# Kernel optimization log

Measured on AMD Instinct MI355X. Metric: run time of the kernel, lower is better.

## Reference

```python
import jax, jax.numpy as jnp
import numpy as np

# module config (matches init_kwargs)
SLICE_W, SLICE_H = 32, 32
STRIDE, WIDTH_INIT = 8, 8
EMBED_DIM = 512
B, H, W = 64, 32, 4096
PAD = (SLICE_W - WIDTH_INIT) // 2  # 12, width padding with constant value 1.0


def setup_inputs() -> dict:
    key = jax.random.key(0)
    k1, k2, k3, k4, k5 = jax.random.split(key, 5)
    u = lambda k, s: jax.random.uniform(k, s, jnp.float32, -0.08, 0.08)
    return {
        "images": jax.random.normal(k1, (B, 1, H, W), jnp.float32),
        "conv_w": u(k2, (1, 1, 3, 3)),          # Conv2d(1,1,3x3) weight (OIHW)
        "conv_b": u(k3, (1,)),
        "lin_w": u(k4, (SLICE_W * SLICE_H, EMBED_DIM)),  # bridge Linear, stored [in,out]
        "lin_b": u(k5, (EMBED_DIM,)),
    }


def reference(images, conv_w, conv_b, lin_w, lin_b):
    b = images.shape[0]
    # pad width with constant 1 (F.pad(..., 'constant', 1))
    padded = jnp.pad(images, ((0, 0), (0, 0), (0, 0), (PAD, PAD)), constant_values=1.0)
    # vectorized replacement of the python loop over stride positions
    starts = np.arange(0, W - 1, STRIDE)               # [S] static
    S = starts.shape[0]                                # 512
    idx = starts[:, None] + np.arange(SLICE_W)[None, :]  # [S, slice_w]
    sl = padded[:, :, :, idx]                          # [B,1,H,S,slice_w]
    sl = jnp.transpose(sl, (0, 3, 1, 2, 4))            # [B,S,1,H,slice_w]
    x = sl.reshape(b * S, 1, H, SLICE_W)               # pixels
    # embedder: Conv2d(1,1,k=3,pad=1) + ReLU
    y = jax.lax.conv_general_dilated(x, conv_w, (1, 1), ((1, 1), (1, 1)))
    y = jax.nn.relu(y + conv_b[None, :, None, None])
    # bridge: Linear(slice_w*slice_h -> embed_dim)
    flat = y.reshape(b * S, H * SLICE_W)
    out = flat @ lin_w + lin_b
    return out.reshape(b, S, EMBED_DIM)
```

## Files before the change

kernel.cpp:

```cpp
#include <hip/hip_runtime.h>
#include <cstdint>
#include <cstddef>

typedef unsigned short u16;
typedef unsigned int   u32;
typedef __attribute__((ext_vector_type(4))) float  f32x4;
typedef __attribute__((ext_vector_type(2))) float  f32x2;
typedef __attribute__((ext_vector_type(2))) u32    u32x2;
typedef __attribute__((ext_vector_type(8))) __bf16 bf16x8;

#define PSW   1056
#define ASTR  72
#define CFW   4128
#define WIN   2080

#define WS_BT  0u
#define WS_CF  1048576u
#define WS_AB  (1048576u + 16908288u)
#define WS_NEED (1048576u + 16908288u + 4194304u)

static __device__ __forceinline__ float b2f(u32 u) {
  union { u32 i; float f; } c; c.i = u << 16; return c.f;
}
static __device__ __forceinline__ u16 f2b(float f) {
  union { float f; u32 i; } c; c.f = f;
  return (u16)((c.i + 0x7FFFu + ((c.i >> 16) & 1u)) >> 16);
}

static __device__ __forceinline__ void gl_lds16(const void* g, void* l) {
  __builtin_amdgcn_global_load_lds(
      (__attribute__((address_space(1))) unsigned int*)(void*)g,
      (__attribute__((address_space(3))) unsigned int*)l, 16, 0, 0);
}
static __device__ __forceinline__ void gl_lds4(const void* g, void* l) {
  __builtin_amdgcn_global_load_lds(
      (__attribute__((address_space(1))) unsigned int*)(void*)g,
      (__attribute__((address_space(3))) unsigned int*)l, 4, 0, 0);
}

__global__ __launch_bounds__(256) void transpose_w(const float* __restrict__ lw,
                                                   u16* __restrict__ bt) {
  __shared__ u16 tile[64][65];
  const int t  = threadIdx.x;
  const int c  = t & 63, r0 = t >> 6;
  const int n0 = blockIdx.x * 64;
  const int k0 = blockIdx.y * 64;
#pragma unroll
  for (int rr = 0; rr < 16; ++rr) {
    const int r = r0 * 16 + rr;
    tile[r][c] = f2b(lw[(size_t)(k0 + r) * 512 + n0 + c]);
  }
  __syncthreads();
#pragma unroll
  for (int rr = 0; rr < 16; ++rr) {
    const int r = r0 * 16 + rr;
    bt[(size_t)(n0 + r) * 1024 + k0 + c] = tile[c][r];
  }
}

__global__ __launch_bounds__(512) void prep2(
    const float* __restrict__ img, const float* __restrict__ cw,
    const float* __restrict__ cb, u16* __restrict__ cf, u32* __restrict__ ab,
    const float* __restrict__ lw, u16* __restrict__ bt)
{
  __shared__ __align__(16) float RING[4 * WIN];
  const int t  = threadIdx.x;
  const int id = blockIdx.x;

  if (id >= 512) {
    u16* tile = (u16*)&RING[0];
    const int c = t & 63, r0 = t >> 6;
    for (int q = 0; q < 16; ++q) {
      const int T  = (id - 512) * 16 + q;
      const int n0 = (T & 7) << 6, k0 = (T >> 3) << 6;
      __syncthreads();
#pragma unroll
      for (int rr = 0; rr < 8; ++rr) {
        const int r = r0 * 8 + rr;
        tile[r * 65 + c] = f2b(lw[(size_t)(k0 + r) * 512 + n0 + c]);
      }
      __syncthreads();
#pragma unroll
      for (int rr = 0; rr < 8; ++rr) {
        const int r = r0 * 8 + rr;
        bt[(size_t)(n0 + r) * 1024 + k0 + c] = tile[c * 65 + r];
      }
    }
    return;
  }

  const int b  = id >> 3, sub = id & 7;
  const int ch = sub & 1, hq = sub >> 1;
  const int h0 = hq << 3;
  const int col0   = ch ? 2032 : 0;
  const int wstart = ch ? 0 : 16;
  const float* imgb = img + (size_t)b * 32 * 4096;

  float w9[9];
#pragma unroll
  for (int q = 0; q < 9; ++q) w9[q] = cw[q];
  const float bias = cb[0];

  auto STAGE = [&](int i2) {
    float* sp = RING + (i2 & 3) * WIN;
    const int hh = h0 - 1 + i2;
    if (hh >= 0 && hh <= 31) {
      const float* src = imgb + (ptrdiff_t)hh * 4096 + col0;
      gl_lds16(src + 4 * t, sp + wstart + ((t >> 6) << 8));
      if (t < 4) gl_lds16(src + 2048 + 4 * t, sp + wstart + 2048);
      if (ch == 0) { if (t < 16) sp[t] = (t < 4) ? 0.0f : 1.0f; }
      else         { if (t < 16) sp[2064 + t] = (t < 12) ? 1.0f : 0.0f; }
    } else {
      *(f32x4*)(sp + (t << 2)) = (f32x4)0.0f;
      if (t < 8) *(f32x4*)(sp + 2048 + (t << 2)) = (f32x4)0.0f;
    }
  };

  STAGE(0); STAGE(1); STAGE(2);
  __syncthreads();

#pragma unroll 1
  for (int it = 0; it < 8; ++it) {
    if (it < 7) STAGE(3 + it);
    const int h = h0 + it;
    const float* R0 = RING + ((it)     & 3) * WIN;
    const float* R1 = RING + ((it + 1) & 3) * WIN;
    const float* R2 = RING + ((it + 2) & 3) * WIN;
    u16* cfrow = cf + (size_t)(b * 32 + h) * CFW;

    f32x4 aa0, aa1, aa2;
    auto CONV4 = [&](int tl, bool exp) {
      const int w4 = tl << 2;
      const f32x4 a0 = *(const f32x4*)(R0 + w4), b0 = *(const f32x4*)(R0 + w4 + 4);
      const float c0 = R0[w4 + 8];
      const f32x4 a1 = *(const f32x4*)(R1 + w4), b1 = *(const f32x4*)(R1 + w4 + 4);
      const float c1 = R1[w4 + 8];
      const f32x4 a2 = *(const f32x4*)(R2 + w4), b2 = *(const f32x4*)(R2 + w4 + 4);
      const float c2 = R2[w4 + 8];
      float o0 = bias, o1 = bias, o2 = bias, o3 = bias;
      o0 += w9[0] * a0.w + w9[1] * b0.x + w9[2] * b0.y;
      o1 += w9[0] * b0.x + w9[1] * b0.y + w9[2] * b0.z;
      o2 += w9[0] * b0.y + w9[1] * b0.z + w9[2] * b0.w;
      o3 += w9[0] * b0.z + w9[1] * b0.w + w9[2] * c0;
      o0 += w9[3] * a1.w + w9[4] * b1.x + w9[5] * b1.y;
      o1 += w9[3] * b1.x + w9[4] * b1.y + w9[5] * b1.z;
      o2 += w9[3] * b1.y + w9[4] * b1.z + w9[5] * b1.w;
      o3 += w9[3] * b1.z + w9[4] * b1.w + w9[5] * c1;
      o0 += w9[6] * a2.w + w9[7] * b2.x + w9[8] * b2.y;
      o1 += w9[6] * b2.x + w9[7] * b2.y + w9[8] * b2.z;
      o2 += w9[6] * b2.y + w9[7] * b2.z + w9[8] * b2.w;
      o3 += w9[6] * b2.z + w9[7] * b2.w + w9[8] * c2;
      u32x2 pk;
      pk.x = (u32)f2b(fmaxf(o0, 0.f)) | ((u32)f2b(fmaxf(o1, 0.f)) << 16);
      pk.y = (u32)f2b(fmaxf(o2, 0.f)) | ((u32)f2b(fmaxf(o3, 0.f)) << 16);
      *(u32x2*)(cfrow + (ch << 11) + (tl << 2)) = pk;
      if (exp) { aa0 = a0; aa1 = a1; aa2 = a2; }
    };

    CONV4(t, true);
    if (ch == 1) {
      if (t < 6) CONV4(512 + t, false);
      if (t == 0) { u32x2 z; z.x = 0u; z.y = 0u; *(u32x2*)(cfrow + 4120) = z; }
    }

    u16* abh = (u16*)ab + (size_t)(b * 32 + h) * 1024;
    if (t & 1) {
      const int j = t >> 1;
      float v = bias;
      v += w9[1] * aa0.x + w9[2] * aa0.y;
      v += w9[4] * aa1.x + w9[5] * aa1.y;
      v += w9[7] * aa2.x + w9[8] * aa2.y;
      abh[((ch << 8) + j) << 1] = f2b(fmaxf(v, 0.f));
    } else if (t >= 8) {
      const int j = (t - 8) >> 1;
      float v = bias;
      v += w9[0] * aa0.z + w9[1] * aa0.w;
      v += w9[3] * aa1.z + w9[4] * aa1.w;
      v += w9[6] * aa2.z + w9[7] * aa2.w;
      abh[(((ch << 8) + j) << 1) | 1] = f2b(fmaxf(v, 0.f));
    } else {
      const int j = 252 + (t >> 1);
      const int wq = 8 * j + 34;
      const f32x2 u0 = *(const f32x2*)(R0 + wq);
      const f32x2 u1 = *(const f32x2*)(R1 + wq);
      const f32x2 u2 = *(const f32x2*)(R2 + wq);
      float v = bias;
      v += w9[0] * u0.x + w9[1] * u0.y;
      v += w9[3] * u1.x + w9[4] * u1.y;
      v += w9[6] * u2.x + w9[7] * u2.y;
      abh[(((ch << 8) + j) << 1) | 1] = f2b(fmaxf(v, 0.f));
    }
    __syncthreads();
  }
}

__global__ __launch_bounds__(256) void gemm_k2(
    const u16* __restrict__ cf, const u32* __restrict__ ab,
    const u16* __restrict__ bt, const float* __restrict__ lb,
    float* __restrict__ out)
{
  __shared__ __align__(16) char sm[2176 + 512 + 16384];
  u16* Ps   = (u16*)sm;
  u32* Ab32 = (u32*)(sm + 2176);
  u16* Bs   = (u16*)(sm + 2688);
  float* Cs = (float*)sm;

  const int t  = threadIdx.x;
  const int orig = blockIdx.y * 4 + blockIdx.x;
  const int wg   = ((orig & 7) << 8) + (orig >> 3);
  const int nt = wg & 3, mt = wg >> 2;
  const int b  = mt >> 3, sg = mt & 7;
  const int n0 = nt << 7;
  const int w  = t >> 6, i = t & 63;
  const int wr = w >> 1, wc = w & 1;
  const int lq = i >> 4, lr = i & 15;

  const int cB = (i & 7) ^ ((i >> 3) & 7);
  const u16* btp = bt + (size_t)(n0 + (w << 5) + (i >> 3)) * 1024 + (cB << 3);
  u16* BsW = Bs + (w << 11);

  const int rP  = (t >= 68) ? 1 : 0;
  const int ccP = t - 68 * rP;
  const u16* cfp = cf + (size_t)(b * 32 + rP) * CFW + (sg << 9) + (ccP << 3);
  u16* PsW = (u16*)((char*)Ps + (w << 10));

  const u32* abp = ab + (size_t)(b * 32 + (t >> 6)) * 512 + (sg << 6) + (t & 63);
  u32* AbW = Ab32 + (w << 6);

  f32x4 acc[2][4];
#pragma unroll
  for (int a = 0; a < 2; ++a)
#pragma unroll
    for (int c = 0; c < 4; ++c) acc[a][c] = (f32x4)0.0f;

  for (int kk = 0; kk < 16; ++kk) {
    __syncthreads();
    gl_lds16(btp,              BsW);
    gl_lds16(btp +  8 * 1024,  BsW + 512);
    gl_lds16(btp + 16 * 1024,  BsW + 1024);
    gl_lds16(btp + 24 * 1024,  BsW + 1536);
    if (t < 136) gl_lds16(cfp, PsW);
    if (t < 128) gl_lds4(abp, AbW);
    btp += 64; cfp += 2 * CFW; abp += 1024;
    __syncthreads();

#pragma unroll
    for (int kc = 0; kc < 2; ++kc) {
      const int bswz = (((kc << 2) + lq) ^ (lr & 7)) << 3;
      bf16x8 af[2], bfv[4];
#pragma unroll
      for (int im = 0; im < 2; ++im) {
        const int ml = wr * 32 + im * 16 + lr;
        af[im] = __builtin_bit_cast(bf16x8,
            *(const uint4*)(Ps + kc * 544 + ((ml + lq) << 3)));
        const u32 a32 = Ab32[kc * 64 + ml];
        union { u16 u; __bf16 h; } lo, hi;
        lo.u = (u16)(a32 & 0xffffu); hi.u = (u16)(a32 >> 16);
        if (lq == 0) af[im][0] = lo.h;
        if (lq == 3) af[im][7] = hi.h;
      }
#pragma unroll
      for (int jn = 0; jn < 4; ++jn) {
        const int n = wc * 64 + jn * 16 + lr;
        bfv[jn] = __builtin_bit_cast(bf16x8, *(const uint4*)(Bs + (n << 6) + bswz));
      }
#pragma unroll
      for (int im = 0; im < 2; ++im)
#pragma unroll
        for (int jn = 0; jn < 4; ++jn)
          acc[im][jn] = __builtin_amdgcn_mfma_f32_16x16x32_bf16(
              af[im], bfv[jn], acc[im][jn], 0, 0, 0);
    }
  }

  float lbv[4];
#pragma unroll
  for (int jn = 0; jn < 4; ++jn) lbv[jn] = lb[n0 + wc * 64 + jn * 16 + lr];

  const int erow = t >> 3, ecol = (t & 7) << 4;
  const int grow_base = (mt << 6) + ((erow >> 4) * 32) + (erow & 15);

#pragma unroll
  for (int im = 0; im < 2; ++im) {
    __syncthreads();
#pragma unroll
    for (int jn = 0; jn < 4; ++jn) {
      const int cl = wc * 64 + jn * 16 + lr;
#pragma unroll
      for (int r = 0; r < 4; ++r)
        Cs[(wr * 16 + lq * 4 + r) * 132 + cl] = acc[im][jn][r] + lbv[jn];
    }
    __syncthreads();
    const size_t grow = (size_t)(grow_base + im * 16);
    float* orow = out + grow * 512 + n0 + ecol;
    const float* crow = Cs + erow * 132 + ecol;
#pragma unroll
    for (int p = 0; p < 4; ++p)
      *(f32x4*)(orow + p * 4) = *(const f32x4*)(crow + p * 4);
  }
}

__global__ __launch_bounds__(256) void fused_fallback(
    const float* __restrict__ img, const float* __restrict__ cw,
    const float* __restrict__ cb, const u16* __restrict__ bt,
    const float* __restrict__ lb, float* __restrict__ out)
{
  __shared__ __align__(16) u16 Ps[4 * PSW];
  __shared__ __align__(16) u16 As[128 * ASTR];
  __shared__ __align__(16) u16 Bs[128 * ASTR];
  const int t = threadIdx.x, nt = blockIdx.x, mt = blockIdx.y;
  const int b = mt >> 2, s0 = (mt & 3) << 7, X0 = s0 << 3, n0 = nt << 7;
  const float* imgb = img + (size_t)b * 32 * 4096;
  float cwf[9];
#pragma unroll
  for (int q = 0; q < 9; ++q) cwf[q] = cw[q];
  const float bias = cb[0];
  const int wv = t >> 6, l = t & 63;
  const int wr = wv >> 1, wc = wv & 1, lq = l >> 4, lr = l & 15;
  const int sl = t >> 1, hsel = t & 1;
  f32x4 acc[4][4];
#pragma unroll
  for (int a = 0; a < 4; ++a)
#pragma unroll
    for (int c = 0; c < 4; ++c) acc[a][c] = (f32x4)0.0f;
  for (int kk = 0; kk < 16; ++kk) {
    const int h0 = kk << 1;
    __syncthreads();
    uint4 bsv[4];
#pragma unroll
    for (int p = 0; p < 4; ++p) {
      const int idx8 = t + (p << 8);
      const int n = idx8 >> 3, k8 = idx8 & 7;
      bsv[p] = *(const uint4*)(bt + (size_t)(n0 + n) * 1024 + (kk << 6) + (k8 << 3));
    }
    for (int idx = t; idx < 4 * PSW; idx += 256) {
      const int r = idx / PSW, xi = idx - r * PSW;
      const int h = h0 - 1 + r, x = X0 - 1 + xi;
      u16 v = 0;
      if (h >= 0 && h < 32 && x >= 0 && x < 4120)
        v = (x < 12 || x >= 4108) ? (u16)0x3F80 : f2b(imgb[h * 4096 + (x - 12)]);
      Ps[idx] = v;
    }
    __syncthreads();
    {
      const int pbase = (sl << 3);
#pragma unroll
      for (int wb = 0; wb < 32; wb += 16) {
        float o[16];
#pragma unroll
        for (int j = 0; j < 16; ++j) o[j] = bias;
#pragma unroll
        for (int dr = 0; dr < 3; ++dr) {
          const u16* p = Ps + (hsel + dr) * PSW + pbase + wb;
          const uint4 va = *(const uint4*)p;
          const uint4 vb = *(const uint4*)(p + 8);
          const u32   vc = *(const u32*)(p + 16);
          float win[18];
          win[0] = b2f(va.x & 0xffffu); win[1] = b2f(va.x >> 16);
          win[2] = b2f(va.y & 0xffffu); win[3] = b2f(va.y >> 16);
          win[4] = b2f(va.z & 0xffffu); win[5] = b2f(va.z >> 16);
          win[6] = b2f(va.w & 0xffffu); win[7] = b2f(va.w >> 16);
          win[8] = b2f(vb.x & 0xffffu); win[9] = b2f(vb.x >> 16);
          win[10] = b2f(vb.y & 0xffffu); win[11] = b2f(vb.y >> 16);
          win[12] = b2f(vb.z & 0xffffu); win[13] = b2f(vb.z >> 16);
          win[14] = b2f(vb.w & 0xffffu); win[15] = b2f(vb.w >> 16);
          win[16] = b2f(vc & 0xffffu);   win[17] = b2f(vc >> 16);
          if (wb == 0) win[0] = 0.f; else win[17] = 0.f;
          const float w0 = cwf[dr * 3], w1 = cwf[dr * 3 + 1], w2 = cwf[dr * 3 + 2];
#pragma unroll
          for (int j = 0; j < 16; ++j)
            o[j] += w0 * win[j] + w1 * win[j + 1] + w2 * win[j + 2];
        }
        u32 pk[8];
#pragma unroll
        for (int q = 0; q < 8; ++q)
          pk[q] = (u32)f2b(fmaxf(o[2 * q], 0.f)) | ((u32)f2b(fmaxf(o[2 * q + 1], 0.f)) << 16);
        uint4* dst = (uint4*)(As + sl * ASTR + (hsel << 5) + wb);
        dst[0] = make_uint4(pk[0], pk[1], pk[2], pk[3]);
        dst[1] = make_uint4(pk[4], pk[5], pk[6], pk[7]);
      }
    }
#pragma unroll
    for (int p = 0; p < 4; ++p) {
      const int idx8 = t + (p << 8);
      const int n = idx8 >> 3, k8 = idx8 & 7;
      *(uint4*)(Bs + n * ASTR + (k8 << 3)) = bsv[p];
    }
    __syncthreads();
#pragma unroll
    for (int kc = 0; kc < 2; ++kc) {
      const int ko = (kc << 5) + (lq << 3);
      bf16x8 af[4], bfv[4];
#pragma unroll
      for (int im = 0; im < 4; ++im)
        af[im] = __builtin_bit_cast(bf16x8,
            *(const uint4*)(As + (wr * 64 + im * 16 + lr) * ASTR + ko));
#pragma unroll
      for (int jn = 0; jn < 4; ++jn)
        bfv[jn] = __builtin_bit_cast(bf16x8,
            *(const uint4*)(Bs + (wc * 64 + jn * 16 + lr) * ASTR + ko));
#pragma unroll
      for (int im = 0; im < 4; ++im)
#pragma unroll
        for (int jn = 0; jn < 4; ++jn)
          acc[im][jn] = __builtin_amdgcn_mfma_f32_16x16x32_bf16(
              af[im], bfv[jn], acc[im][jn], 0, 0, 0);
    }
  }
#pragma unroll
  for (int jn = 0; jn < 4; ++jn) {
    const int col = n0 + wc * 64 + jn * 16 + lr;
    const float lbv = lb[col];
#pragma unroll
    for (int im = 0; im < 4; ++im) {
      const int row0 = (mt << 7) + wr * 64 + im * 16 + (lq << 2);
#pragma unroll
      for (int r = 0; r < 4; ++r)
        out[(size_t)(row0 + r) * 512 + col] = acc[im][jn][r] + lbv;
    }
  }
}

extern "C" void kernel_launch(void* const* d_in, const int* in_sizes, int n_in,
                              void* d_out, int out_size, void* d_ws, size_t ws_size,
                              hipStream_t stream) {
  const float* img = (const float*)d_in[0];
  const float* cw  = (const float*)d_in[1];
  const float* cb  = (const float*)d_in[2];
  const float* lw  = (const float*)d_in[3];
  const float* lb  = (const float*)d_in[4];
  float* out = (float*)d_out;

  u16* btw = (u16*)((char*)d_ws + WS_BT);

  if (ws_size >= WS_NEED) {
    u16* cfp = (u16*)((char*)d_ws + WS_CF);
    u32* abp = (u32*)((char*)d_ws + WS_AB);
    prep2<<<dim3(520), 512, 0, stream>>>(img, cw, cb, cfp, abp, lw, btw);
    gemm_k2<<<dim3(4, 512), 256, 0, stream>>>(cfp, abp, btw, lb, out);
  } else {
    transpose_w<<<dim3(8, 16), 256, 0, stream>>>(lw, btw);
    fused_fallback<<<dim3(4, 256), 256, 0, stream>>>(img, cw, cb, btw, lb, out);
  }
}
```

Before: 153.9 us.

## Replace LDS ring-buffered conv prep with one-row-per-block direct global loads

The prep kernel no longer stages image rows through a four-slot LDS ring with async global-to-LDS loads and per-row barriers. Instead each 256-thread block computes a single output row, and every thread reads its 3x16 input window straight from global memory with vector loads. This gives far more, smaller blocks (2056 instead of 520), removes the barrier-bound pipeline, and computes the boundary-column outputs directly. The cost is redundant input reads across neighbouring rows, which now rely on the cache, plus per-element padding logic at the edges.

New measurement: 219.8 us. 1.43x slower.

```diff
diff --git a/kernel.cpp b/kernel.cpp
--- a/kernel.cpp
+++ b/kernel.cpp
@@ -12,7 +12,6 @@
 #define PSW   1056
 #define ASTR  72
 #define CFW   4128
-#define WIN   2080
 
 #define WS_BT  0u
 #define WS_CF  1048576u
@@ -58,139 +57,108 @@
   }
 }
 
-__global__ __launch_bounds__(512) void prep2(
+__global__ __launch_bounds__(256) void prep3(
     const float* __restrict__ img, const float* __restrict__ cw,
     const float* __restrict__ cb, u16* __restrict__ cf, u32* __restrict__ ab,
     const float* __restrict__ lw, u16* __restrict__ bt)
 {
-  __shared__ __align__(16) float RING[4 * WIN];
+  __shared__ __align__(16) u16 tile[64 * 65];
   const int t  = threadIdx.x;
   const int id = blockIdx.x;
 
-  if (id >= 512) {
-    u16* tile = (u16*)&RING[0];
+  if (id >= 2048) {
     const int c = t & 63, r0 = t >> 6;
     for (int q = 0; q < 16; ++q) {
-      const int T  = (id - 512) * 16 + q;
+      const int T  = (id - 2048) * 16 + q;
       const int n0 = (T & 7) << 6, k0 = (T >> 3) << 6;
       __syncthreads();
 #pragma unroll
-      for (int rr = 0; rr < 8; ++rr) {
-        const int r = r0 * 8 + rr;
+      for (int rr = 0; rr < 16; ++rr) {
+        const int r = r0 * 16 + rr;
         tile[r * 65 + c] = f2b(lw[(size_t)(k0 + r) * 512 + n0 + c]);
       }
       __syncthreads();
 #pragma unroll
-      for (int rr = 0; rr < 8; ++rr) {
-        const int r = r0 * 8 + rr;
+      for (int rr = 0; rr < 16; ++rr) {
+        const int r = r0 * 16 + rr;
         bt[(size_t)(n0 + r) * 1024 + k0 + c] = tile[c * 65 + r];
       }
     }
     return;
   }
 
-  const int b  = id >> 3, sub = id & 7;
-  const int ch = sub & 1, hq = sub >> 1;
-  const int h0 = hq << 3;
-  const int col0   = ch ? 2032 : 0;
-  const int wstart = ch ? 0 : 16;
-  const float* imgb = img + (size_t)b * 32 * 4096;
-
+  const int wg = ((id & 7) << 8) + (id >> 3);
+  const int bb = wg >> 5, hh = wg & 31;
+  const float* imgb = img + (size_t)bb * 32 * 4096;
   float w9[9];
 #pragma unroll
   for (int q = 0; q < 9; ++q) w9[q] = cw[q];
   const float bias = cb[0];
 
-  auto STAGE = [&](int i2) {
-    float* sp = RING + (i2 & 3) * WIN;
-    const int hh = h0 - 1 + i2;
-    if (hh >= 0 && hh <= 31) {
-      const float* src = imgb + (ptrdiff_t)hh * 4096 + col0;
-      gl_lds16(src + 4 * t, sp + wstart + ((t >> 6) << 8));
-      if (t < 4) gl_lds16(src + 2048 + 4 * t, sp + wstart + 2048);
-      if (ch == 0) { if (t < 16) sp[t] = (t < 4) ? 0.0f : 1.0f; }
-      else         { if (t < 16) sp[2064 + t] = (t < 12) ? 1.0f : 0.0f; }
-    } else {
-      *(f32x4*)(sp + (t << 2)) = (f32x4)0.0f;
-      if (t < 8) *(f32x4*)(sp + 2048 + (t << 2)) = (f32x4)0.0f;
-    }
+  u16* cfrow = cf + (size_t)(bb * 32 + hh) * CFW;
+
+  auto CONV8 = [&](int c) {
+    float o[8];
+#pragma unroll
+    for (int j = 0; j < 8; ++j) o[j] = bias;
+#pragma unroll
+    for (int dr = 0; dr < 3; ++dr) {
+      const int hr = hh - 1 + dr;
+      if (hr < 0 || hr > 31) continue;
+      const float* rp = imgb + (ptrdiff_t)hr * 4096;
+      float win[16];
+      if (c >= 2 && c < 512) {
+        const f32x4* vp = (const f32x4*)(rp + (c << 3) - 16);
+        *(f32x4*)&win[0]  = vp[0];
+        *(f32x4*)&win[4]  = vp[1];
+        *(f32x4*)&win[8]  = vp[2];
+        *(f32x4*)&win[12] = vp[3];
+      } else {
+#pragma unroll
+        for (int k2 = 0; k2 < 16; ++k2) {
+          const int p  = (c << 3) - 4 + k2;
+          int ci = p - 12; ci = ci < 0 ? 0 : (ci > 4095 ? 4095 : ci);
+          const float v = rp[ci];
+          win[k2] = (p < 12) ? 1.0f : (p >= 4120 ? 0.0f : (p >= 4108 ? 1.0f : v));
+        }
+      }
+      const float w0 = w9[dr * 3], w1 = w9[dr * 3 + 1], w2 = w9[dr * 3 + 2];
+#pragma unroll
+      for (int j = 0; j < 8; ++j)
+        o[j] += w0 * win[j + 3] + w1 * win[j + 4] + w2 * win[j + 5];
+    }
+    u32 pk[4];
+#pragma unroll
+    for (int q = 0; q < 4; ++q)
+      pk[q] = (u32)f2b(fmaxf(o[2 * q], 0.f)) |
+              ((u32)f2b(fmaxf(o[2 * q + 1], 0.f)) << 16);
+    *(uint4*)(cfrow + (c << 3)) = make_uint4(pk[0], pk[1], pk[2], pk[3]);
   };
 
-  STAGE(0); STAGE(1); STAGE(2);
-  __syncthreads();
-
-#pragma unroll 1
-  for (int it = 0; it < 8; ++it) {
-    if (it < 7) STAGE(3 + it);
-    const int h = h0 + it;
-    const float* R0 = RING + ((it)     & 3) * WIN;
-    const float* R1 = RING + ((it + 1) & 3) * WIN;
-    const float* R2 = RING + ((it + 2) & 3) * WIN;
-    u16* cfrow = cf + (size_t)(b * 32 + h) * CFW;
-
-    f32x4 aa0, aa1, aa2;
-    auto CONV4 = [&](int tl, bool exp) {
-      const int w4 = tl << 2;
-      const f32x4 a0 = *(const f32x4*)(R0 + w4), b0 = *(const f32x4*)(R0 + w4 + 4);
-      const float c0 = R0[w4 + 8];
-      const f32x4 a1 = *(const f32x4*)(R1 + w4), b1 = *(const f32x4*)(R1 + w4 + 4);
-      const float c1 = R1[w4 + 8];
-      const f32x4 a2 = *(const f32x4*)(R2 + w4), b2 = *(const f32x4*)(R2 + w4 + 4);
-      const float c2 = R2[w4 + 8];
-      float o0 = bias, o1 = bias, o2 = bias, o3 = bias;
-      o0 += w9[0] * a0.w + w9[1] * b0.x + w9[2] * b0.y;
-      o1 += w9[0] * b0.x + w9[1] * b0.y + w9[2] * b0.z;
-      o2 += w9[0] * b0.y + w9[1] * b0.z + w9[2] * b0.w;
-      o3 += w9[0] * b0.z + w9[1] * b0.w + w9[2] * c0;
-      o0 += w9[3] * a1.w + w9[4] * b1.x + w9[5] * b1.y;
-      o1 += w9[3] * b1.x + w9[4] * b1.y + w9[5] * b1.z;
-      o2 += w9[3] * b1.y + w9[4] * b1.z + w9[5] * b1.w;
-      o3 += w9[3] * b1.z + w9[4] * b1.w + w9[5] * c1;
-      o0 += w9[6] * a2.w + w9[7] * b2.x + w9[8] * b2.y;
-      o1 += w9[6] * b2.x + w9[7] * b2.y + w9[8] * b2.z;
-      o2 += w9[6] * b2.y + w9[7] * b2.z + w9[8] * b2.w;
-      o3 += w9[6] * b2.z + w9[7] * b2.w + w9[8] * c2;
-      u32x2 pk;
-      pk.x = (u32)f2b(fmaxf(o0, 0.f)) | ((u32)f2b(fmaxf(o1, 0.f)) << 16);
-      pk.y = (u32)f2b(fmaxf(o2, 0.f)) | ((u32)f2b(fmaxf(o3, 0.f)) << 16);
-      *(u32x2*)(cfrow + (ch << 11) + (tl << 2)) = pk;
-      if (exp) { aa0 = a0; aa1 = a1; aa2 = a2; }
-    };
-
-    CONV4(t, true);
-    if (ch == 1) {
-      if (t < 6) CONV4(512 + t, false);
-      if (t == 0) { u32x2 z; z.x = 0u; z.y = 0u; *(u32x2*)(cfrow + 4120) = z; }
-    }
-
-    u16* abh = (u16*)ab + (size_t)(b * 32 + h) * 1024;
-    if (t & 1) {
-      const int j = t >> 1;
-      float v = bias;
-      v += w9[1] * aa0.x + w9[2] * aa0.y;
-      v += w9[4] * aa1.x + w9[5] * aa1.y;
-      v += w9[7] * aa2.x + w9[8] * aa2.y;
-      abh[((ch << 8) + j) << 1] = f2b(fmaxf(v, 0.f));
-    } else if (t >= 8) {
-      const int j = (t - 8) >> 1;
-      float v = bias;
-      v += w9[0] * aa0.z + w9[1] * aa0.w;
-      v += w9[3] * aa1.z + w9[4] * aa1.w;
-      v += w9[6] * aa2.z + w9[7] * aa2.w;
-      abh[(((ch << 8) + j) << 1) | 1] = f2b(fmaxf(v, 0.f));
-    } else {
-      const int j = 252 + (t >> 1);
-      const int wq = 8 * j + 34;
-      const f32x2 u0 = *(const f32x2*)(R0 + wq);
-      const f32x2 u1 = *(const f32x2*)(R1 + wq);
-      const f32x2 u2 = *(const f32x2*)(R2 + wq);
-      float v = bias;
-      v += w9[0] * u0.x + w9[1] * u0.y;
-      v += w9[3] * u1.x + w9[4] * u1.y;
-      v += w9[6] * u2.x + w9[7] * u2.y;
-      abh[(((ch << 8) + j) << 1) | 1] = f2b(fmaxf(v, 0.f));
-    }
-    __syncthreads();
+  CONV8(t);
+  CONV8(t + 256);
+  if (t < 3) CONV8(512 + t);
+  if (t == 3) *(uint4*)(cfrow + 4120) = make_uint4(0u, 0u, 0u, 0u);
+
+  u32* abrow = ab + (size_t)(bb * 32 + hh) * 512;
+#pragma unroll
+  for (int ss = 0; ss < 2; ++ss) {
+    const int s = t + (ss << 8);
+    float o0 = bias, o1 = bias;
+#pragma unroll
+    for (int dr = 0; dr < 3; ++dr) {
+      const int hr = hh - 1 + dr;
+      if (hr < 0 || hr > 31) continue;
+      const float* rp = imgb + (ptrdiff_t)hr * 4096;
+      float p0, p1, q0, q1;
+      if (s >= 2)   { f32x2 v = *(const f32x2*)(rp + (s << 3) - 12); p0 = v.x; p1 = v.y; }
+      else          { p0 = 1.0f; p1 = 1.0f; }
+      if (s <= 509) { f32x2 v = *(const f32x2*)(rp + (s << 3) + 18); q0 = v.x; q1 = v.y; }
+      else          { q0 = 1.0f; q1 = 1.0f; }
+      o0 += w9[dr * 3 + 1] * p0 + w9[dr * 3 + 2] * p1;
+      o1 += w9[dr * 3]     * q0 + w9[dr * 3 + 1] * q1;
+    }
+    abrow[s] = (u32)f2b(fmaxf(o0, 0.f)) | ((u32)f2b(fmaxf(o1, 0.f)) << 16);
   }
 }
 
@@ -436,7 +404,7 @@
   if (ws_size >= WS_NEED) {
     u16* cfp = (u16*)((char*)d_ws + WS_CF);
     u32* abp = (u32*)((char*)d_ws + WS_AB);
-    prep2<<<dim3(520), 512, 0, stream>>>(img, cw, cb, cfp, abp, lw, btw);
+    prep3<<<dim3(2056), 256, 0, stream>>>(img, cw, cb, cfp, abp, lw, btw);
     gemm_k2<<<dim3(4, 512), 256, 0, stream>>>(cfp, abp, btw, lb, out);
   } else {
     transpose_w<<<dim3(8, 16), 256, 0, stream>>>(lw, btw);
```
